# Optimization experiments

Hardware: AMD Instinct MI355X
Metric: run time of the kernel (lower is better)

## Reference

```python
import jax, jax.numpy as jnp
import numpy as np

# Surrogate-gradient spike (ActFun_adp from DH-SNN): Heaviside fwd, multi-Gaussian bwd
GAMMA, LENS, SCALE, HIGHT = 0.5, 0.5, 6.0, 0.15
VTH = 1.0

def _gauss(x, mu, sigma):
    return jnp.exp(-((x - mu) ** 2) / (2.0 * sigma ** 2)) / (jnp.sqrt(2.0 * jnp.pi) * sigma)

@jax.custom_vjp
def spike_fn(x):
    return (x > 0).astype(x.dtype)

def _spike_fwd(x):
    return spike_fn(x), x

def _spike_bwd(x, g):
    temp = (_gauss(x, 0.0, LENS) * (1.0 + HIGHT)
            - _gauss(x, LENS, SCALE * LENS) * HIGHT
            - _gauss(x, -LENS, SCALE * LENS) * HIGHT)
    return (g * temp * GAMMA,)

spike_fn.defvjp(_spike_fwd, _spike_bwd)

B, T, IN, H, OUT = 128, 1000, 700, 512, 20

def setup_inputs() -> dict:
    key = jax.random.key(0)
    ks = jax.random.split(key, 10)
    lim1 = float(1.0 / np.sqrt(IN))
    lim2 = float(1.0 / np.sqrt(H))
    return {
        "x": jax.random.uniform(ks[0], (B, T, IN), jnp.float32),
        "W1": jax.random.uniform(ks[1], (H, IN), jnp.float32, -lim1, lim1),
        "b1": jax.random.uniform(ks[2], (H,), jnp.float32, -lim1, lim1),
        "tau_m1": jax.random.uniform(ks[3], (H,), jnp.float32, 0.0, 4.0),
        "tau_n1": jax.random.uniform(ks[4], (H,), jnp.float32, 0.0, 4.0),
        "W2": jax.random.uniform(ks[5], (OUT, H), jnp.float32, -lim2, lim2),
        "b2": jax.random.uniform(ks[6], (OUT,), jnp.float32, -lim2, lim2),
        "tau_m2": jax.random.uniform(ks[7], (OUT,), jnp.float32, 0.0, 4.0),
        "mem1_0": jax.random.uniform(ks[8], (B, H), jnp.float32),   # set_neuron_state uses rand init
        "mem2_0": jax.random.uniform(ks[9], (B, OUT), jnp.float32),
    }

def reference(x, W1, b1, tau_m1, tau_n1, W2, b2, tau_m2, mem1_0, mem2_0):
    alpha1 = jax.nn.sigmoid(tau_m1)   # [H] membrane decay
    beta1 = jax.nn.sigmoid(tau_n1)    # [H] dendritic decay (branch=1 -> branch dim collapsed)
    alpha2 = jax.nn.sigmoid(tau_m2)   # [OUT] readout decay
    # Input projection is time-invariant: one big GEMM instead of T small ones.
    proj = jnp.einsum('bti,hi->bth', x, W1) + b1  # [B,T,H]

    def step(carry, p_t):
        mem1, spike1, d_in, mem2 = carry
        d_in = beta1 * d_in + (1.0 - beta1) * p_t                       # dendritic filter
        mem1 = mem1 * alpha1 + (1.0 - alpha1) * d_in - VTH * spike1      # LIF soft reset
        spike1 = spike_fn(mem1 - VTH)
        mem2 = mem2 * alpha2 + (1.0 - alpha2) * (spike1 @ W2.T + b2)     # leaky readout
        return (mem1, spike1, d_in, mem2), mem2

    init = (mem1_0, jnp.zeros_like(mem1_0), jnp.zeros_like(mem1_0), mem2_0)
    _, outs = jax.lax.scan(step, init, jnp.swapaxes(proj, 0, 1))  # scan over time
    return jnp.swapaxes(outs, 0, 1)  # [B, T, OUT]
```

## Files before the change

kernel.cpp:

```cpp
#include <hip/hip_runtime.h>
#include <stdint.h>

#define Bd   128
#define Td   1000
#define INd  700
#define Hd   512
#define OUTd 20
#define Md   (Bd * Td)
#define KPAD 704
#define KIT  22
#define KH   1408

typedef _Float16 f16;
typedef f16 f16x4 __attribute__((ext_vector_type(4)));
typedef f16 f16x8 __attribute__((ext_vector_type(8)));
typedef float f32x4 __attribute__((ext_vector_type(4)));

__device__ __forceinline__ void gld_lds16(const void* g, void* l) {
  __builtin_amdgcn_global_load_lds(
      (__attribute__((address_space(1))) void*)(g),
      (__attribute__((address_space(3))) void*)(l), 16, 0, 0);
}

__global__ __launch_bounds__(256) void pack_kernel(
    const float* __restrict__ src, f16* __restrict__ dst, int nrows) {
  const int t = blockIdx.x * 256 + threadIdx.x;
  if (t >= nrows * 88) return;
  const int m = t / 88;
  const int rem = t - m * 88;
  const int kt = rem >> 2;
  const int lc = rem & 3;
  const int k0 = kt * 32 + lc * 8;
  const float* sp = src + (size_t)m * INd + k0;
  float v[8];
  if (k0 + 8 <= INd) {
    const float4 v0 = *(const float4*)sp;
    const float4 v1 = *(const float4*)(sp + 4);
    v[0] = v0.x; v[1] = v0.y; v[2] = v0.z; v[3] = v0.w;
    v[4] = v1.x; v[5] = v1.y; v[6] = v1.z; v[7] = v1.w;
  } else {
#pragma unroll
    for (int u = 0; u < 8; ++u) v[u] = (k0 + u < INd) ? sp[u] : 0.f;
  }
  f16x8 h1, h2;
#pragma unroll
  for (int u = 0; u < 8; ++u) {
    const f16 a = (f16)v[u];
    h1[u] = a;
    h2[u] = (f16)(v[u] - (float)a);
  }
  const int s = m & 7;
  f16* out = dst + (size_t)m * KH + (size_t)kt * 64;
  *(f16x8*)(out + ((lc ^ s) << 3)) = h1;
  *(f16x8*)(out + (((lc + 4) ^ s) << 3)) = h2;
}

#define SBAR __builtin_amdgcn_sched_barrier(0)

#define LOAD_FRAGS(S, MH, NH, AB, BB)                                   \
  _Pragma("unroll")                                                     \
  for (int mi = 0; mi < 4; ++mi) {                                      \
    const int rb = (wm0 + (MH) * 64 + mi * 16 + fr) << 6;               \
    a1##S[mi] = *(const f16x8*)&(AB)[rb + o1];                          \
    a2##S[mi] = *(const f16x8*)&(AB)[rb + o2];                          \
  }                                                                     \
  _Pragma("unroll")                                                     \
  for (int nj = 0; nj < 2; ++nj) {                                      \
    const int cb = (wn0 + (NH) * 32 + nj * 16 + fr) << 6;               \
    b1##S[nj] = *(const f16x8*)&(BB)[cb + o1];                          \
    b2##S[nj] = *(const f16x8*)&(BB)[cb + o2];                          \
  }

#define MFMA_PHASE(S, MH, NH)                                           \
  __builtin_amdgcn_s_setprio(1);                                        \
  _Pragma("unroll")                                                     \
  for (int mi = 0; mi < 4; ++mi)                                        \
  _Pragma("unroll")                                                     \
  for (int nj = 0; nj < 2; ++nj) {                                      \
    f32x4 a = acc[(MH) * 4 + mi][(NH) * 2 + nj];                        \
    a = __builtin_amdgcn_mfma_f32_16x16x32_f16(a1##S[mi], b1##S[nj], a, 0, 0, 0); \
    a = __builtin_amdgcn_mfma_f32_16x16x32_f16(a1##S[mi], b2##S[nj], a, 0, 0, 0); \
    a = __builtin_amdgcn_mfma_f32_16x16x32_f16(a2##S[mi], b1##S[nj], a, 0, 0, 0); \
    acc[(MH) * 4 + mi][(NH) * 2 + nj] = a;                              \
  }                                                                     \
  __builtin_amdgcn_s_setprio(0);

#define STAGE_A(NB, GO)                                                 \
  _Pragma("unroll")                                                     \
  for (int j = 0; j < 4; ++j)                                           \
    gld_lds16(Ag + (size_t)j * (64 * KH) + (GO), &As[NB][tid * 8 + j * 4096]);

#define STAGE_B(NB, GO)                                                 \
  _Pragma("unroll")                                                     \
  for (int j = 0; j < 4; ++j)                                           \
    gld_lds16(Bg + (size_t)j * (64 * KH) + (GO), &Bs[NB][tid * 8 + j * 4096]);

__global__ __launch_bounds__(512, 2) void gemm1_kernel(
    const f16* __restrict__ Xp, const f16* __restrict__ Wp,
    const float* __restrict__ b1, float* __restrict__ proj) {
  __shared__ __align__(16) f16 As[2][256 * 64];
  __shared__ __align__(16) f16 Bs[2][256 * 64];
  const int tid = threadIdx.x;

  const int l = blockIdx.x;
  const int bb = (l & 7) * 125 + (l >> 3);
  const int m0 = (bb >> 1) << 8;
  const int n0 = (bb & 1) << 8;

  const int srow = tid >> 3, sc = tid & 7;
  const f16* Ag = Xp + (size_t)(m0 + srow) * KH + (sc << 3);
  const f16* Bg = Wp + (size_t)(n0 + srow) * KH + (sc << 3);

  const int wv = tid >> 6, lane = tid & 63;
  const int wm0 = (wv >> 2) << 7;
  const int wn0 = (wv & 3) << 6;
  const int fr = lane & 15;
  const int fq = lane >> 4;
  const int swz = (fr & 7) << 4;
  const int o1 = ((fq << 4) ^ swz) >> 1;
  const int o2 = (((fq + 4) << 4) ^ swz) >> 1;

  f32x4 acc[8][4];
#pragma unroll
  for (int i = 0; i < 8; ++i)
#pragma unroll
    for (int j = 0; j < 4; ++j) acc[i][j] = (f32x4){0.f, 0.f, 0.f, 0.f};

  f16x8 a1E[4], a2E[4], b1E[2], b2E[2];
  f16x8 a1O[4], a2O[4], b1O[2], b2O[2];

  STAGE_A(0, 0);
  STAGE_B(0, 0);
  asm volatile("s_waitcnt vmcnt(0)" ::: "memory");
  __builtin_amdgcn_sched_barrier(0);
  __builtin_amdgcn_s_barrier();
  LOAD_FRAGS(E, 0, 0, As[0], Bs[0]);

#pragma unroll 1
  for (int t = 0; t < KIT; ++t) {
    const f16* Ac = As[t & 1];
    const f16* Bc = Bs[t & 1];
    const int nb = (t & 1) ^ 1;
    const bool pf = (t + 1 < KIT);
    const size_t go = (size_t)(t + 1) << 6;

    LOAD_FRAGS(O, 0, 1, Ac, Bc);
    if (pf) { STAGE_A(nb, go); }
    SBAR;
    MFMA_PHASE(E, 0, 0);
    SBAR;
    LOAD_FRAGS(E, 1, 0, Ac, Bc);
    if (pf) { STAGE_B(nb, go); }
    SBAR;
    MFMA_PHASE(O, 0, 1);
    SBAR;
    LOAD_FRAGS(O, 1, 1, Ac, Bc);
    SBAR;
    MFMA_PHASE(E, 1, 0);
    SBAR;
    if (pf) {
      asm volatile("s_waitcnt vmcnt(0) lgkmcnt(0)" ::: "memory");
      __builtin_amdgcn_sched_barrier(0);
      __builtin_amdgcn_s_barrier();
      LOAD_FRAGS(E, 0, 0, As[nb], Bs[nb]);
    }
    SBAR;
    MFMA_PHASE(O, 1, 1);
    SBAR;
  }

#pragma unroll
  for (int ni = 0; ni < 4; ++ni) {
    const int n = n0 + wn0 + ni * 16 + fr;
    const float bias = b1[n];
#pragma unroll
    for (int mi = 0; mi < 8; ++mi) {
      const int mb = m0 + wm0 + mi * 16 + (fq << 2);
      float* p = proj + (size_t)mb * Hd + n;
#pragma unroll
      for (int rr = 0; rr < 4; ++rr)
        p[(size_t)rr * Hd] = acc[mi][ni][rr] + bias;
    }
  }
}

__global__ __launch_bounds__(256) void w1split_kernel(
    const float* __restrict__ W1, f16* __restrict__ W1a,
    f16* __restrict__ W1b) {
  const int idx = blockIdx.x * 256 + threadIdx.x;
  if (idx >= 512 * KPAD) return;
  const int n = idx / KPAD, k = idx - n * KPAD;
  const float v = (k < INd) ? W1[n * INd + k] : 0.f;
  const f16 h1 = (f16)v;
  const f16 h2 = (f16)(v - (float)h1);
  W1a[idx] = h1;
  W1b[idx] = h2;
}

__global__ __launch_bounds__(256) void gemm1_fb_kernel(
    const float* __restrict__ X, const f16* __restrict__ W1a,
    const f16* __restrict__ W1b, const float* __restrict__ b1,
    float* __restrict__ proj) {
  __shared__ __align__(16) f16 A1s[128 * 40];
  __shared__ __align__(16) f16 A2s[128 * 40];
  __shared__ __align__(16) f16 B1s[128 * 40];
  __shared__ __align__(16) f16 B2s[128 * 40];

  const int tid = threadIdx.x;
  const int n0 = blockIdx.x * 128;
  const int m0 = blockIdx.y * 128;

  const int srow = tid >> 1;
  const int skq  = (tid & 1) << 4;

  const float* Xp  = X + (size_t)(m0 + srow) * INd;
  const f16*   Bap = W1a + (size_t)(n0 + srow) * KPAD + skq;
  const f16*   Bbp = W1b + (size_t)(n0 + srow) * KPAD + skq;

  const int wv = tid >> 6, lane = tid & 63;
  const int wm0 = (wv >> 1) * 64, wn0 = (wv & 1) * 64;
  const int fr = lane & 15;
  const int fq = lane >> 4;

  f32x4 acc[4][4];
#pragma unroll
  for (int i = 0; i < 4; ++i)
#pragma unroll
    for (int j = 0; j < 4; ++j) acc[i][j] = (f32x4){0.f, 0.f, 0.f, 0.f};

  const float4 z4 = make_float4(0.f, 0.f, 0.f, 0.f);
  float4 ax[4];
  f16x8 bq1[2], bq2[2];

#pragma unroll
  for (int i = 0; i < 4; ++i) ax[i] = *(const float4*)(Xp + skq + 4 * i);
  bq1[0] = *(const f16x8*)(Bap);     bq1[1] = *(const f16x8*)(Bap + 8);
  bq2[0] = *(const f16x8*)(Bbp);     bq2[1] = *(const f16x8*)(Bbp + 8);

#pragma unroll 1
  for (int it = 0; it < KIT; ++it) {
    __syncthreads();
#pragma unroll
    for (int i = 0; i < 4; ++i) {
      const float4 v = ax[i];
      f16x4 h1, h2;
      h1.x = (f16)v.x; h2.x = (f16)(v.x - (float)h1.x);
      h1.y = (f16)v.y; h2.y = (f16)(v.y - (float)h1.y);
      h1.z = (f16)v.z; h2.z = (f16)(v.z - (float)h1.z);
      h1.w = (f16)v.w; h2.w = (f16)(v.w - (float)h1.w);
      *(f16x4*)&A1s[srow * 40 + skq + 4 * i] = h1;
      *(f16x4*)&A2s[srow * 40 + skq + 4 * i] = h2;
    }
    *(f16x8*)&B1s[srow * 40 + skq]     = bq1[0];
    *(f16x8*)&B1s[srow * 40 + skq + 8] = bq1[1];
    *(f16x8*)&B2s[srow * 40 + skq]     = bq2[0];
    *(f16x8*)&B2s[srow * 40 + skq + 8] = bq2[1];
    __syncthreads();
    if (it + 1 < KIT) {
      const int k0 = (it + 1) * 32;
#pragma unroll
      for (int i = 0; i < 4; ++i) {
        const int k = k0 + skq + 4 * i;
        ax[i] = (k + 4 <= INd) ? *(const float4*)(Xp + k) : z4;
      }
      bq1[0] = *(const f16x8*)(Bap + k0);
      bq1[1] = *(const f16x8*)(Bap + k0 + 8);
      bq2[0] = *(const f16x8*)(Bbp + k0);
      bq2[1] = *(const f16x8*)(Bbp + k0 + 8);
    }
    f16x8 a1f[4], a2f[4], b1f[4], b2f[4];
#pragma unroll
    for (int mi = 0; mi < 4; ++mi) {
      const int off = (wm0 + mi * 16 + fr) * 40 + fq * 8;
      a1f[mi] = *(const f16x8*)&A1s[off];
      a2f[mi] = *(const f16x8*)&A2s[off];
    }
#pragma unroll
    for (int ni = 0; ni < 4; ++ni) {
      const int off = (wn0 + ni * 16 + fr) * 40 + fq * 8;
      b1f[ni] = *(const f16x8*)&B1s[off];
      b2f[ni] = *(const f16x8*)&B2s[off];
    }
#pragma unroll
    for (int mi = 0; mi < 4; ++mi)
#pragma unroll
      for (int ni = 0; ni < 4; ++ni) {
        acc[mi][ni] = __builtin_amdgcn_mfma_f32_16x16x32_f16(
            a1f[mi], b1f[ni], acc[mi][ni], 0, 0, 0);
        acc[mi][ni] = __builtin_amdgcn_mfma_f32_16x16x32_f16(
            a1f[mi], b2f[ni], acc[mi][ni], 0, 0, 0);
        acc[mi][ni] = __builtin_amdgcn_mfma_f32_16x16x32_f16(
            a2f[mi], b1f[ni], acc[mi][ni], 0, 0, 0);
      }
  }

#pragma unroll
  for (int ni = 0; ni < 4; ++ni) {
    const int n = n0 + wn0 + ni * 16 + fr;
    const float bias = b1[n];
#pragma unroll
    for (int mi = 0; mi < 4; ++mi) {
      const int mb = m0 + wm0 + mi * 16 + fq * 4;
      float* p = proj + (size_t)mb * Hd + n;
#pragma unroll
      for (int r = 0; r < 4; ++r)
        p[(size_t)r * Hd] = acc[mi][ni][r] + bias;
    }
  }
}

#define S1_PHASE(QC, QN, T0)                                      \
  {                                                               \
    const int tp_ = (T0) + 24;                                    \
    _Pragma("unroll")                                             \
    for (int u = 0; u < 8; ++u) {                                 \
      const int tt = (tp_ + u < Td) ? (tp_ + u) : (Td - 1);       \
      buf[QN][u] = pp[(size_t)tt * Hd];                           \
    }                                                             \
    _Pragma("unroll")                                             \
    for (int u = 0; u < 8; ++u) {                                 \
      const float pv = buf[QC][u];                                \
      d = bn * d + ombn * pv;                                     \
      mem = am * mem + omam * d - s;                              \
      const bool fire = mem > 1.0f;                               \
      s = fire ? 1.f : 0.f;                                       \
      const unsigned long long msk = __ballot(fire);              \
      if (lane == 0) sp[(size_t)((T0) + u) * 8] = msk;            \
    }                                                             \
  }

__global__ __launch_bounds__(256) void scan1_kernel(
    const float* __restrict__ proj, const float* __restrict__ tau_m1,
    const float* __restrict__ tau_n1, const float* __restrict__ mem1_0,
    unsigned long long* __restrict__ spk) {
  const int gid = blockIdx.x * 256 + threadIdx.x;
  const int b = gid >> 9;
  const int h = gid & 511;
  const float am = 1.f / (1.f + expf(-tau_m1[h]));
  const float bn = 1.f / (1.f + expf(-tau_n1[h]));
  const float omam = 1.f - am, ombn = 1.f - bn;
  float mem = mem1_0[(b << 9) | h];
  float d = 0.f, s = 0.f;
  const float* pp = proj + (size_t)b * Td * Hd + h;
  unsigned long long* sp = spk + (size_t)b * Td * 8 + (h >> 6);
  const int lane = threadIdx.x & 63;

  float buf[4][8];
#pragma unroll
  for (int q = 0; q < 3; ++q)
#pragma unroll
    for (int u = 0; u < 8; ++u)
      buf[q][u] = pp[(size_t)(q * 8 + u) * Hd];

#pragma unroll 1
  for (int t0 = 0; t0 < 992; t0 += 32) {
    S1_PHASE(0, 3, t0);
    S1_PHASE(1, 0, t0 + 8);
    S1_PHASE(2, 1, t0 + 16);
    S1_PHASE(3, 2, t0 + 24);
  }
  S1_PHASE(0, 3, 992);
}

__global__ __launch_bounds__(256) void gemm2_kernel(
    const unsigned long long* __restrict__ spk, const float* __restrict__ W2,
    const float* __restrict__ b2, float* __restrict__ R, int Mtotal) {
  __shared__ float W2s[Hd * OUTd];
  const int tid = threadIdx.x;
  for (int idx = tid; idx < Hd * OUTd; idx += 256) {
    const int h = idx / OUTd, o = idx - h * OUTd;
    W2s[idx] = W2[o * Hd + h];
  }
  __syncthreads();
  const int wave = tid >> 6, lane = tid & 63;
  const int mg = lane / OUTd;
  const int o = lane - mg * OUTd;
  if (mg >= 3) return;
  const float bias = b2[o];
  const int mbase = blockIdx.x * 96 + wave * 24 + mg;
#pragma unroll 1
  for (int i = 0; i < 8; ++i) {
    const int m = mbase + i * 3;
    if (m >= Mtotal) break;
    float r = bias;
    const unsigned long long* mp = spk + (size_t)m * 8;
#pragma unroll
    for (int c = 0; c < 8; ++c) {
      unsigned long long mask = mp[c];
      const float* wrow = W2s + (c << 6) * OUTd + o;
      while (mask) {
        const int j = __builtin_ctzll(mask);
        mask &= mask - 1;
        r += wrow[j * OUTd];
      }
    }
    R[(size_t)m * OUTd + o] = r;
  }
}

__global__ __launch_bounds__(256) void scan2_kernel(
    const float* __restrict__ R, const float* __restrict__ tau_m2,
    const float* __restrict__ mem2_0, float* __restrict__ out) {
  __shared__ float leS[8][20];
  __shared__ float stS[8][20];
  const int b = blockIdx.x;
  const int tid = threadIdx.x;
  const int c = tid / OUTd;
  const int o = tid - c * OUTd;
  const bool active = tid < 160;
  float a2 = 0.f, oma2 = 0.f;
  if (active) {
    a2 = 1.f / (1.f + expf(-tau_m2[o]));
    oma2 = 1.f - a2;
  }
  const float* Rb = R + (size_t)b * Td * OUTd;
  float* Ob = out + (size_t)b * Td * OUTd;
  const int t0 = c * 125;

  if (active) {
    float m = 0.f;
    for (int u = 0; u < 125; ++u)
      m = a2 * m + oma2 * Rb[(size_t)(t0 + u) * OUTd + o];
    leS[c][o] = m;
  }
  __syncthreads();
  if (tid < OUTd) {
    const float a = 1.f / (1.f + expf(-tau_m2[tid]));
    float aL = 1.f;
    for (int i = 0; i < 125; ++i) aL *= a;
    float m = mem2_0[b * OUTd + tid];
    for (int cc = 0; cc < 8; ++cc) {
      stS[cc][tid] = m;
      m = aL * m + leS[cc][tid];
    }
  }
  __syncthreads();
  if (active) {
    float m = stS[c][o];
    for (int u = 0; u < 125; ++u) {
      m = a2 * m + oma2 * Rb[(size_t)(t0 + u) * OUTd + o];
      Ob[(size_t)(t0 + u) * OUTd + o] = m;
    }
  }
}

extern "C" void kernel_launch(void* const* d_in, const int* in_sizes, int n_in,
                              void* d_out, int out_size, void* d_ws, size_t ws_size,
                              hipStream_t stream) {
  const float* x      = (const float*)d_in[0];
  const float* W1     = (const float*)d_in[1];
  const float* b1     = (const float*)d_in[2];
  const float* tau_m1 = (const float*)d_in[3];
  const float* tau_n1 = (const float*)d_in[4];
  const float* W2     = (const float*)d_in[5];
  const float* b2     = (const float*)d_in[6];
  const float* tau_m2 = (const float*)d_in[7];
  const float* mem1_0 = (const float*)d_in[8];
  const float* mem2_0 = (const float*)d_in[9];
  float* out = (float*)d_out;

  const size_t proj_b = (size_t)Md * Hd * sizeof(float);
  const size_t xp_b   = (size_t)Md * KH * sizeof(f16);
  const size_t wp_b   = (size_t)512 * KH * sizeof(f16);
  const size_t spk_b  = (size_t)Md * 8 * sizeof(unsigned long long);

  float* proj = (float*)d_ws;

  if (ws_size >= proj_b + xp_b + wp_b) {
    f16* Xpk = (f16*)((char*)d_ws + proj_b);
    f16* Wpk = (f16*)((char*)d_ws + proj_b + xp_b);
    unsigned long long* spk = (unsigned long long*)((char*)d_ws + proj_b);
    float* R = (float*)((char*)d_ws + proj_b + spk_b);

    pack_kernel<<<dim3(Md * 88 / 256), 256, 0, stream>>>(x, Xpk, Md);
    pack_kernel<<<dim3(512 * 88 / 256), 256, 0, stream>>>(W1, Wpk, 512);
    gemm1_kernel<<<dim3((Hd / 256) * (Md / 256)), 512, 0, stream>>>(Xpk, Wpk,
                                                                    b1, proj);
    scan1_kernel<<<dim3(Bd * Hd / 256), 256, 0, stream>>>(proj, tau_m1, tau_n1,
                                                          mem1_0, spk);
    gemm2_kernel<<<dim3((Md + 95) / 96), 256, 0, stream>>>(spk, W2, b2, R, Md);
    scan2_kernel<<<dim3(Bd), 256, 0, stream>>>(R, tau_m2, mem2_0, out);
  } else {
    unsigned long long* spk =
        (unsigned long long*)((char*)d_ws + proj_b);
    float* R = (float*)((char*)spk + spk_b);
    f16* W1a = (f16*)R;
    f16* W1b = W1a + 512 * KPAD;

    w1split_kernel<<<dim3((512 * KPAD + 255) / 256), 256, 0, stream>>>(W1, W1a,
                                                                       W1b);
    gemm1_fb_kernel<<<dim3(Hd / 128, Md / 128), 256, 0, stream>>>(x, W1a, W1b,
                                                                  b1, proj);
    scan1_kernel<<<dim3(Bd * Hd / 256), 256, 0, stream>>>(proj, tau_m1, tau_n1,
                                                          mem1_0, spk);
    gemm2_kernel<<<dim3((Md + 95) / 96), 256, 0, stream>>>(spk, W2, b2, R, Md);
    scan2_kernel<<<dim3(Bd), 256, 0, stream>>>(R, tau_m2, mem2_0, out);
  }
}
```

Before: 926.6 us.

## Deepen scan1 prefetch, hoist spike mask loads, merge pack launches

The scan1 kernel's register prefetch ring grows from 4 to 8 stages, so loads of proj are issued 56 timesteps ahead instead of 24. This is meant to hide more global memory latency in the sequential scan, at the cost of more registers per thread. gemm2 now loads all eight spike mask words for a row before walking their set bits, so the loads are not serialized behind the loops. The two pack kernel launches for x and W1 are merged into a single launch to save one launch.

```diff
diff --git a/kernel.cpp b/kernel.cpp
--- a/kernel.cpp
+++ b/kernel.cpp
@@ -23,9 +23,19 @@
 }
 
 __global__ __launch_bounds__(256) void pack_kernel(
-    const float* __restrict__ src, f16* __restrict__ dst, int nrows) {
-  const int t = blockIdx.x * 256 + threadIdx.x;
-  if (t >= nrows * 88) return;
+    const float* __restrict__ x, const float* __restrict__ W1,
+    f16* __restrict__ Xp, f16* __restrict__ Wp) {
+  int t = blockIdx.x * 256 + threadIdx.x;
+  const int xcnt = Md * 88;
+  const float* src;
+  f16* dst;
+  if (t < xcnt) {
+    src = x; dst = Xp;
+  } else {
+    t -= xcnt;
+    if (t >= 512 * 88) return;
+    src = W1; dst = Wp;
+  }
   const int m = t / 88;
   const int rem = t - m * 88;
   const int kt = rem >> 2;
@@ -311,7 +321,7 @@
 
 #define S1_PHASE(QC, QN, T0)                                      \
   {                                                               \
-    const int tp_ = (T0) + 24;                                    \
+    const int tp_ = (T0) + 56;                                    \
     _Pragma("unroll")                                             \
     for (int u = 0; u < 8; ++u) {                                 \
       const int tt = (tp_ + u < Td) ? (tp_ + u) : (Td - 1);       \
@@ -345,21 +355,29 @@
   unsigned long long* sp = spk + (size_t)b * Td * 8 + (h >> 6);
   const int lane = threadIdx.x & 63;
 
-  float buf[4][8];
-#pragma unroll
-  for (int q = 0; q < 3; ++q)
+  float buf[8][8];
+#pragma unroll
+  for (int q = 0; q < 7; ++q)
 #pragma unroll
     for (int u = 0; u < 8; ++u)
       buf[q][u] = pp[(size_t)(q * 8 + u) * Hd];
 
 #pragma unroll 1
-  for (int t0 = 0; t0 < 992; t0 += 32) {
-    S1_PHASE(0, 3, t0);
+  for (int t0 = 0; t0 < 960; t0 += 64) {
+    S1_PHASE(0, 7, t0);
     S1_PHASE(1, 0, t0 + 8);
     S1_PHASE(2, 1, t0 + 16);
     S1_PHASE(3, 2, t0 + 24);
-  }
-  S1_PHASE(0, 3, 992);
+    S1_PHASE(4, 3, t0 + 32);
+    S1_PHASE(5, 4, t0 + 40);
+    S1_PHASE(6, 5, t0 + 48);
+    S1_PHASE(7, 6, t0 + 56);
+  }
+  S1_PHASE(0, 7, 960);
+  S1_PHASE(1, 0, 968);
+  S1_PHASE(2, 1, 976);
+  S1_PHASE(3, 2, 984);
+  S1_PHASE(4, 3, 992);
 }
 
 __global__ __launch_bounds__(256) void gemm2_kernel(
@@ -382,11 +400,14 @@
   for (int i = 0; i < 8; ++i) {
     const int m = mbase + i * 3;
     if (m >= Mtotal) break;
+    const unsigned long long* mp = spk + (size_t)m * 8;
+    unsigned long long mk[8];
+#pragma unroll
+    for (int c = 0; c < 8; ++c) mk[c] = mp[c];
     float r = bias;
-    const unsigned long long* mp = spk + (size_t)m * 8;
 #pragma unroll
     for (int c = 0; c < 8; ++c) {
-      unsigned long long mask = mp[c];
+      unsigned long long mask = mk[c];
       const float* wrow = W2s + (c << 6) * OUTd + o;
       while (mask) {
         const int j = __builtin_ctzll(mask);
@@ -472,8 +493,8 @@
     unsigned long long* spk = (unsigned long long*)((char*)d_ws + proj_b);
     float* R = (float*)((char*)d_ws + proj_b + spk_b);
 
-    pack_kernel<<<dim3(Md * 88 / 256), 256, 0, stream>>>(x, Xpk, Md);
-    pack_kernel<<<dim3(512 * 88 / 256), 256, 0, stream>>>(W1, Wpk, 512);
+    pack_kernel<<<dim3(((Md + 512) * 88 + 255) / 256), 256, 0, stream>>>(
+        x, W1, Xpk, Wpk);
     gemm1_kernel<<<dim3((Hd / 256) * (Md / 256)), 512, 0, stream>>>(Xpk, Wpk,
                                                                     b1, proj);
     scan1_kernel<<<dim3(Bd * Hd / 256), 256, 0, stream>>>(proj, tau_m1, tau_n1,
```

New measurement: 894.2 us. 1.04x faster.
